# Optimization experiments

Hardware: AMD Instinct MI355X
Metric: run time of the kernel (lower is better)

Reference implementation:

```python
import jax, jax.numpy as jnp
import numpy as np

EPS = 1e-4      # MovingBatchNorm eps
STEPS = 3       # fixed RK4 steps standing in for adaptive dopri5
B, N, D, C, H = 4, 2048, 3, 64, 512


def setup_inputs() -> dict:
    key = jax.random.key(0)
    ks = iter(jax.random.split(key, 40))
    f32 = jnp.float32

    def rn(shape, s=1.0):
        return jax.random.normal(next(ks), shape, dtype=f32) * s

    inp = {}
    inp['x'] = rn((B, N, D))
    inp['c'] = rn((B, N, C))
    for p in ('bn1', 'bn2'):
        inp[p + '_mean'] = rn((D,), 0.1)
        inp[p + '_var'] = jax.random.uniform(next(ks), (D,), dtype=f32, minval=0.5, maxval=1.5)
        inp[p + '_log_gamma'] = jnp.zeros((D,), f32)
        inp[p + '_beta'] = jnp.zeros((D,), f32)
    inp['sqrt_T'] = jnp.array([np.sqrt(0.5)], f32)  # train_T: T = sqrt_T**2
    dims = [(D, H), (H, H), (H, H), (H, D)]  # concatsquash (in, out)
    for i, (din, dout) in enumerate(dims):
        inp[f'W{i}'] = rn((dout, din), 0.05)
        inp[f'b{i}'] = jnp.zeros((dout,), f32)
        inp[f'Wg{i}'] = rn((dout, C + 1), 0.05)
        inp[f'bg{i}'] = jnp.zeros((dout,), f32)
        inp[f'Wb{i}'] = rn((dout, C + 1), 0.05)
    return inp


def _odenet(t, x, c, layers):
    # ConcatSquash MLP: lin(x)*sigmoid(hyper_gate([t,c])) + hyper_bias([t,c])
    ctx = jnp.concatenate([jnp.broadcast_to(t, c.shape[:-1] + (1,)).astype(x.dtype), c], axis=-1)
    h = x
    for i, (W, b, Wg, bg, Wb) in enumerate(layers):
        h = (h @ W.T + b) * jax.nn.sigmoid(ctx @ Wg.T + bg) + ctx @ Wb.T
        if i < len(layers) - 1:
            h = jnp.tanh(h)
    return h


def _aug_dyn(t, x, c, layers):
    # augmented CNF dynamics: (dx/dt, dlogp/dt) with exact divergence via D jvps
    f = lambda xx: _odenet(t, xx, c, layers)
    div = jnp.zeros(x.shape[:-1] + (1,), x.dtype)
    dx = None
    for i in range(x.shape[-1]):
        e = jnp.zeros_like(x).at[..., i].set(1.0)
        dx, jv = jax.jvp(f, (x,), (e,))
        div = div + jv[..., i:i + 1]
    return dx, -div


def _rk4(x0, lp0, c, layers, T):
    dt = T / STEPS

    def step(carry, i):
        x, lp = carry
        t = i.astype(x.dtype) * dt
        k1x, k1l = _aug_dyn(t, x, c, layers)
        k2x, k2l = _aug_dyn(t + 0.5 * dt, x + 0.5 * dt * k1x, c, layers)
        k3x, k3l = _aug_dyn(t + 0.5 * dt, x + 0.5 * dt * k2x, c, layers)
        k4x, k4l = _aug_dyn(t + dt, x + dt * k3x, c, layers)
        x = x + (dt / 6.0) * (k1x + 2.0 * k2x + 2.0 * k3x + k4x)
        lp = lp + (dt / 6.0) * (k1l + 2.0 * k2l + 2.0 * k3l + k4l)
        return (x, lp), None

    (x, lp), _ = jax.lax.scan(step, (x0, lp0), jnp.arange(STEPS))
    return x, lp


def _bn(x, lp, mean, var, log_gamma, beta):
    # MovingBatchNorm1d, eval mode; logdet = sum(log_gamma - 0.5*log(var+eps))
    y = (x - mean) * jnp.exp(log_gamma) / jnp.sqrt(var + EPS) + beta
    ld = jnp.sum(log_gamma - 0.5 * jnp.log(var + EPS))
    return y, lp - ld


def reference(x, c, bn1_mean, bn1_var, bn1_log_gamma, bn1_beta,
              bn2_mean, bn2_var, bn2_log_gamma, bn2_beta, sqrt_T,
              W0, b0, Wg0, bg0, Wb0, W1, b1, Wg1, bg1, Wb1,
              W2, b2, Wg2, bg2, Wb2, W3, b3, Wg3, bg3, Wb3):
    layers = [(W0, b0, Wg0, bg0, Wb0), (W1, b1, Wg1, bg1, Wb1),
              (W2, b2, Wg2, bg2, Wb2), (W3, b3, Wg3, bg3, Wb3)]
    lp = jnp.zeros(x.shape[:-1] + (1,), x.dtype)  # (B,N,1)
    x, lp = _bn(x, lp, bn1_mean, bn1_var, bn1_log_gamma, bn1_beta)
    T = sqrt_T[0] ** 2
    x, lp = _rk4(x, lp, c, layers, T)
    x, lp = _bn(x, lp, bn2_mean, bn2_var, bn2_log_gamma, bn2_beta)
    return x, jnp.sum(lp, axis=(1, 2))
```

## Files before the change

### kernel.cpp

```cpp
#include <hip/hip_runtime.h>
#include <hip/hip_fp8.h>

#define PTS 8192
#define HDIM 512
#define BN_EPS 1e-4f
#define HSTRB 528
#define TS 256.0f
#define SCL1 0x7f7f7f7f

typedef unsigned short u16;
typedef unsigned char u8;
typedef long long i64;
typedef u16 u16x8 __attribute__((ext_vector_type(8)));
typedef short s16x8 __attribute__((ext_vector_type(8)));
typedef float f32x4 __attribute__((ext_vector_type(4)));
typedef float f32x2 __attribute__((ext_vector_type(2)));
typedef int i32x4 __attribute__((ext_vector_type(4)));
typedef int i32x8 __attribute__((ext_vector_type(8)));

__device__ __forceinline__ float bf2f(u16 u) {
  unsigned x = ((unsigned)u) << 16;
  return __builtin_bit_cast(float, x);
}
__device__ __forceinline__ u16 f2bf(float f) {
  unsigned x = __builtin_bit_cast(unsigned, f);
  x += 0x7fffu + ((x >> 16) & 1u);
  return (u16)(x >> 16);
}
__device__ __forceinline__ u8 f2f8(float x) {
  int v = __builtin_amdgcn_cvt_pk_fp8_f32(x, x, 0, false);
  return (u8)(v & 0xff);
}
__device__ __forceinline__ unsigned pk4_f8(float a, float b, float c, float d) {
  int v = __builtin_amdgcn_cvt_pk_fp8_f32(a, b, 0, false);
  v = __builtin_amdgcn_cvt_pk_fp8_f32(c, d, v, true);
  return (unsigned)v;
}
__device__ __forceinline__ float sigf(float x) {
  return __builtin_amdgcn_rcpf(1.f + __expf(-x));
}
__device__ __forceinline__ float fast_tanh(float x) {
  float e = __expf(2.f * x);
  return 1.f - 2.f * __builtin_amdgcn_rcpf(e + 1.f);
}
__device__ __forceinline__ void gl2lds16(const u16* g, u16* l) {
  __builtin_amdgcn_global_load_lds(
      (const __attribute__((address_space(1))) void*)g,
      (__attribute__((address_space(3))) void*)l, 16, 0, 0);
}
__device__ __forceinline__ i32x8 ld32(const u8* p) {
  i32x4 lo = *(const i32x4*)p;
  i32x4 hi = *(const i32x4*)(p + 16);
  return __builtin_shufflevector(lo, hi, 0, 1, 2, 3, 4, 5, 6, 7);
}

#define MFMA_SC(A, B, C) \
  __builtin_amdgcn_mfma_scale_f32_16x16x128_f8f6f4((A), (B), (C), 0, 0, 0, SCL1, 0, SCL1)

#define MX_GEMM(WL, HB)                                                     \
  {                                                                         \
    _Pragma("unroll")                                                       \
    for (int zi = 0; zi < 4; ++zi)                                          \
      _Pragma("unroll")                                                     \
      for (int zj = 0; zj < 4; ++zj)                                        \
        _Pragma("unroll")                                                   \
        for (int zr = 0; zr < 4; ++zr) acc[zi][zj][zr] = 0.f;               \
    const u8* wp = (WL);                                                    \
    _Pragma("unroll 1")                                                     \
    for (int c = 0; c < 4; ++c) {                                           \
      const u8* hc = (HB) + c * 128;                                        \
      i32x8 af0 = ld32(hc);                                                 \
      i32x8 af1 = ld32(hc + (size_t)16 * HSTRB);                            \
      i32x8 af2 = ld32(hc + (size_t)32 * HSTRB);                            \
      i32x8 af3 = ld32(hc + (size_t)48 * HSTRB);                            \
      i32x8 bA = ld32(wp);                                                  \
      i32x8 bB = ld32(wp + 2048);                                           \
      __builtin_amdgcn_sched_barrier(0);                                    \
      __builtin_amdgcn_s_setprio(1);                                        \
      acc[0][0] = MFMA_SC(af0, bA, acc[0][0]);                              \
      acc[1][0] = MFMA_SC(af1, bA, acc[1][0]);                              \
      acc[2][0] = MFMA_SC(af2, bA, acc[2][0]);                              \
      acc[3][0] = MFMA_SC(af3, bA, acc[3][0]);                              \
      acc[0][1] = MFMA_SC(af0, bB, acc[0][1]);                              \
      acc[1][1] = MFMA_SC(af1, bB, acc[1][1]);                              \
      acc[2][1] = MFMA_SC(af2, bB, acc[2][1]);                              \
      acc[3][1] = MFMA_SC(af3, bB, acc[3][1]);                              \
      __builtin_amdgcn_s_setprio(0);                                        \
      __builtin_amdgcn_sched_barrier(0);                                    \
      bA = ld32(wp + 4096);                                                 \
      bB = ld32(wp + 6144);                                                 \
      __builtin_amdgcn_sched_barrier(0);                                    \
      __builtin_amdgcn_s_setprio(1);                                        \
      acc[0][2] = MFMA_SC(af0, bA, acc[0][2]);                              \
      acc[1][2] = MFMA_SC(af1, bA, acc[1][2]);                              \
      acc[2][2] = MFMA_SC(af2, bA, acc[2][2]);                              \
      acc[3][2] = MFMA_SC(af3, bA, acc[3][2]);                              \
      acc[0][3] = MFMA_SC(af0, bB, acc[0][3]);                              \
      acc[1][3] = MFMA_SC(af1, bB, acc[1][3]);                              \
      acc[2][3] = MFMA_SC(af2, bB, acc[2][3]);                              \
      acc[3][3] = MFMA_SC(af3, bB, acc[3][3]);                              \
      __builtin_amdgcn_s_setprio(0);                                        \
      __builtin_amdgcn_sched_barrier(0);                                    \
      wp += 65536;                                                          \
    }                                                                       \
  }

struct PrepArgs {
  const float *W1, *W2;
  u8 *W1s, *W2s;
  const float* c;
  u16* cb;
  const float *Wg0, *Wg1, *Wg2, *Wb0, *Wb1, *Wb2;
  const float *bg0, *bg1, *bg2;
  u16* Wpack;
  float* bias_pack;
  const float *x, *m1, *v1, *lg1, *be1;
  float *x_cur;
  const float *Wg3, *bg3, *Wb3;
  float *G3, *B3;
  const float *W0, *b0, *b1, *b2, *W3;
  float *E0, *E1, *E2;
};
__global__ void prep_kernel(PrepArgs a) {
  int i = blockIdx.x * 256 + threadIdx.x;
  if (i < 512 * 512) {
    int n = i >> 9, k = i & 511;
    int c = k >> 7, q2 = (k >> 5) & 3, b = k & 31;
    int w = n >> 6, j = (n >> 4) & 3, lr = n & 15;
    size_t d = (size_t)c * 65536 + (size_t)w * 8192 + (size_t)j * 2048 +
               (size_t)(q2 * 16 + lr) * 32 + b;
    a.W1s[d] = f2f8(a.W1[i]);
    a.W2s[d] = f2f8(a.W2[i]);
  }
  if (i < PTS * 64) a.cb[i] = f2bf(a.c[i]);
  if (i < 6 * 512 * 64) {
    int sec = i >> 15;
    int within = i & 32767;
    int o = within >> 6, k = within & 63;
    const float* src[6] = {a.Wg0, a.Wg1, a.Wg2, a.Wb0, a.Wb1, a.Wb2};
    a.Wpack[i] = f2bf(src[sec][o * 65 + 1 + k]);
  }
  if (i < 3072) {
    int sec = i >> 9, o = i & 511;
    const float* bgl[3] = {a.bg0, a.bg1, a.bg2};
    a.bias_pack[i] = (sec < 3) ? bgl[sec][o] : 0.f;
  }
  if (i < 512) {
    int o = i;
    a.E0[o * 8 + 0] = a.W0[o * 3];
    a.E0[o * 8 + 1] = a.W0[o * 3 + 1];
    a.E0[o * 8 + 2] = a.W0[o * 3 + 2];
    a.E0[o * 8 + 3] = a.b0[o];
    a.E0[o * 8 + 4] = a.Wg0[o * 65];
    a.E0[o * 8 + 5] = a.Wb0[o * 65];
    a.E0[o * 8 + 6] = 0.f; a.E0[o * 8 + 7] = 0.f;
    a.E1[o * 4 + 0] = a.b1[o];
    a.E1[o * 4 + 1] = a.Wg1[o * 65];
    a.E1[o * 4 + 2] = a.Wb1[o * 65];
    a.E1[o * 4 + 3] = 0.f;
    a.E2[o * 8 + 0] = a.b2[o];
    a.E2[o * 8 + 1] = a.Wg2[o * 65];
    a.E2[o * 8 + 2] = a.Wb2[o * 65];
    a.E2[o * 8 + 3] = a.W3[o];
    a.E2[o * 8 + 4] = a.W3[512 + o];
    a.E2[o * 8 + 5] = a.W3[1024 + o];
    a.E2[o * 8 + 6] = 0.f; a.E2[o * 8 + 7] = 0.f;
  }
  if (i < PTS * 3) {
    int d = i % 3;
    a.x_cur[i] = (a.x[i] - a.m1[d]) * __expf(a.lg1[d]) * rsqrtf(a.v1[d] + BN_EPS) + a.be1[d];
  }
  {
    int lane = threadIdx.x & 63;
    int p = (blockIdx.x * 256 + threadIdx.x) >> 6;
    float cv = a.c[(size_t)p * 64 + lane];
    float ag[3], ab[3];
    #pragma unroll
    for (int o = 0; o < 3; ++o) {
      ag[o] = cv * a.Wg3[o * 65 + 1 + lane];
      ab[o] = cv * a.Wb3[o * 65 + 1 + lane];
    }
    #pragma unroll
    for (int off = 32; off > 0; off >>= 1) {
      #pragma unroll
      for (int o = 0; o < 3; ++o) {
        ag[o] += __shfl_xor(ag[o], off);
        ab[o] += __shfl_xor(ab[o], off);
      }
    }
    if (lane == 0) {
      #pragma unroll
      for (int o = 0; o < 3; ++o) {
        a.G3[p * 3 + o] = ag[o] + a.bg3[o];
        a.B3[p * 3 + o] = ab[o];
      }
    }
  }
}

struct GatesGemmArgs {
  const u16 *A, *W;
  const float* bias;
  u16* GBi;
};
__global__ __launch_bounds__(256) void gates_gemm(GatesGemmArgs a) {
  __shared__ u16 As[128 * 32];
  __shared__ u16 Bs[128 * 32];
  int tid = threadIdx.x;
  int m0 = blockIdx.x * 128, n0 = blockIdx.y * 128;
  int wave = tid >> 6, lane = tid & 63;
  int wm = (wave & 1) * 64, wn = (wave >> 1) * 64;
  int lr = lane & 15, quad = lane >> 4;

  int rowS = tid >> 2, colS = (tid & 3) * 8;
  const u16* gA0 = a.A + (size_t)(m0 + rowS) * 64 + colS;
  const u16* gB0 = a.W + (size_t)(n0 + rowS) * 64 + colS;
  u16* sA0 = &As[tid * 8];
  u16* sA1 = &As[2048 + tid * 8];
  u16* sB0 = &Bs[tid * 8];
  u16* sB1 = &Bs[2048 + tid * 8];

  f32x4 acc[4][4];
  #pragma unroll
  for (int i = 0; i < 4; ++i)
    #pragma unroll
    for (int j = 0; j < 4; ++j)
      #pragma unroll
      for (int r = 0; r < 4; ++r) acc[i][j][r] = 0.f;

  for (int k0 = 0; k0 < 64; k0 += 32) {
    if (k0) __syncthreads();
    gl2lds16(gA0 + k0, sA0);
    gl2lds16(gA0 + (size_t)64 * 64 + k0, sA1);
    gl2lds16(gB0 + k0, sB0);
    gl2lds16(gB0 + (size_t)64 * 64 + k0, sB1);
    __syncthreads();
    s16x8 af[4], bfr[4];
    #pragma unroll
    for (int i = 0; i < 4; ++i)
      af[i] = *(const s16x8*)&As[(wm + i * 16 + lr) * 32 + quad * 8];
    #pragma unroll
    for (int j = 0; j < 4; ++j)
      bfr[j] = *(const s16x8*)&Bs[(wn + j * 16 + lr) * 32 + quad * 8];
    #pragma unroll
    for (int i = 0; i < 4; ++i)
      #pragma unroll
      for (int j = 0; j < 4; ++j)
        acc[i][j] = __builtin_amdgcn_mfma_f32_16x16x32_bf16(af[i], bfr[j], acc[i][j], 0, 0, 0);
  }

  #pragma unroll
  for (int j = 0; j < 4; ++j) {
    int n = n0 + wn + j * 16 + lr;
    int sec = n >> 9, col = n & 511;
    int l = (sec < 3) ? sec : sec - 3;
    int off = col * 2 + ((sec < 3) ? 0 : 1);
    float bv = a.bias[n];
    u16* outp = a.GBi + (size_t)l * PTS * 1024 + off;
    #pragma unroll
    for (int i = 0; i < 4; ++i) {
      int mrow = m0 + wm + i * 16 + quad * 4;
      #pragma unroll
      for (int r = 0; r < 4; ++r)
        outp[(size_t)(mrow + r) * 1024] = f2bf(acc[i][j][r] + bv);
    }
  }
}

struct FlowArgs {
  const float* sqrtT;
  const float *G3, *B3, *Wg3, *Wb3, *b3;
  const float* x0;
  const u16 *GBi0, *GBi1, *GBi2;
  const float *E0, *E1, *E2;
  const u8 *W1s, *W2s;
  const float *m2, *v2, *lg2, *be2;
  float* out_x;
  float* lp_state;
};

__global__ __launch_bounds__(512, 4) void flow_kernel(FlowArgs a) {
  __shared__ __align__(16) u8 HsA[64 * HSTRB];
  __shared__ __align__(16) u8 HsB[64 * HSTRB];
  __shared__ float part[8][16][8];
  __shared__ float xs[2][16][3], kxs[16][3];
  __shared__ float kls[16], lps[16];
  __shared__ float g3s[16][3], b3s[16][3];

  int tid = threadIdx.x;
  int w = tid >> 6, lane = tid & 63, lr = lane & 15, quad = lane >> 4;
  int n0 = w * 64;
  int p0 = blockIdx.x * 16;
  int pl0 = tid >> 5;
  int base_o = (tid & 31) * 16;
  bool desig = (tid & 31) == 0;
  float s0 = a.sqrtT[0];
  float dt = s0 * s0 * (1.f / 3.f);

  const u8* w1l = a.W1s + (size_t)w * 8192 + (size_t)lane * 32;
  const u8* w2l = a.W2s + (size_t)w * 8192 + (size_t)lane * 32;
  const u8* hbA = (const u8*)HsA + (size_t)lr * HSTRB + quad * 32;
  const u8* hbB = (const u8*)HsB + (size_t)lr * HSTRB + quad * 32;

  float wg3r[3], wb3r[3], b3r[3];
  #pragma unroll
  for (int r = 0; r < 3; ++r) {
    wg3r[r] = a.Wg3[r * 65];
    wb3r[r] = a.Wb3[r * 65];
    b3r[r] = a.b3[r];
  }

  const u16* g0p = a.GBi0 + (size_t)(p0 + pl0) * 1024 + 2 * base_o;
  const u16* g1p = a.GBi1 + (size_t)(p0 + quad) * 1024 + 2 * (n0 + lr);
  const u16* g2p = a.GBi2 + (size_t)(p0 + quad) * 1024 + 2 * (n0 + lr);

  if (desig) {
    #pragma unroll
    for (int r = 0; r < 3; ++r) {
      xs[0][pl0][r] = a.x0[(p0 + pl0) * 3 + r];
      g3s[pl0][r] = a.G3[(p0 + pl0) * 3 + r];
      b3s[pl0][r] = a.B3[(p0 + pl0) * 3 + r];
    }
    lps[pl0] = 0.f;
  }
  u16x8 gc0 = *(const u16x8*)(g0p);
  u16x8 gc1 = *(const u16x8*)(g0p + 8);
  u16x8 gc2 = *(const u16x8*)(g0p + 16);
  u16x8 gc3 = *(const u16x8*)(g0p + 24);
  __syncthreads();

  #pragma unroll 1
  for (int s = 0; s < 12; ++s) {
    int sub = s & 3;
    float t = ((float)(s >> 2) + ((sub == 0) ? 0.f : (sub == 3) ? 1.f : 0.5f)) * dt;

    float o0, o1, o2;
    if (s == 0) {
      o0 = xs[0][pl0][0]; o1 = xs[0][pl0][1]; o2 = xs[0][pl0][2];
    } else {
      int m = (s - 1) & 3, q = (s - 1) >> 2;
      float tp = ((float)q + ((m == 0) ? 0.f : (m == 3) ? 1.f : 0.5f)) * dt;
      float fr0 = 0.f, fr1 = 0.f, fr2 = 0.f, fr3 = 0.f, fr4 = 0.f, fr5 = 0.f;
      #pragma unroll
      for (int ww = 0; ww < 8; ++ww) {
        f32x4 pa = *(const f32x4*)&part[ww][pl0][0];
        f32x2 pb = *(const f32x2*)&part[ww][pl0][4];
        fr0 += pa[0]; fr1 += pa[1]; fr2 += pa[2];
        fr3 += pa[3]; fr4 += pb[0]; fr5 += pb[1];
      }
      float ga0 = sigf(g3s[pl0][0] + tp * wg3r[0]);
      float ga1 = sigf(g3s[pl0][1] + tp * wg3r[1]);
      float ga2 = sigf(g3s[pl0][2] + tp * wg3r[2]);
      float dx0 = fmaf(fr0 + b3r[0], ga0, b3s[pl0][0] + tp * wb3r[0]);
      float dx1 = fmaf(fr1 + b3r[1], ga1, b3s[pl0][1] + tp * wb3r[1]);
      float dx2 = fmaf(fr2 + b3r[2], ga2, b3s[pl0][2] + tp * wb3r[2]);
      float klv = -(fr3 * ga0 + fr4 * ga1 + fr5 * ga2);
      float bx0 = xs[q & 1][pl0][0];
      float bx1 = xs[q & 1][pl0][1];
      float bx2 = xs[q & 1][pl0][2];
      if (m == 3) {
        float sc = dt * (1.f / 6.f);
        o0 = bx0 + sc * (kxs[pl0][0] + dx0);
        o1 = bx1 + sc * (kxs[pl0][1] + dx1);
        o2 = bx2 + sc * (kxs[pl0][2] + dx2);
        if (desig) {
          xs[(q + 1) & 1][pl0][0] = o0;
          xs[(q + 1) & 1][pl0][1] = o1;
          xs[(q + 1) & 1][pl0][2] = o2;
          lps[pl0] += sc * (kls[pl0] + klv);
        }
      } else {
        float cf = (m == 2) ? dt : 0.5f * dt;
        o0 = fmaf(cf, dx0, bx0);
        o1 = fmaf(cf, dx1, bx1);
        o2 = fmaf(cf, dx2, bx2);
        if (desig) {
          if (m == 0) {
            kxs[pl0][0] = dx0; kxs[pl0][1] = dx1; kxs[pl0][2] = dx2;
            kls[pl0] = klv;
          } else {
            kxs[pl0][0] += 2.f * dx0; kxs[pl0][1] += 2.f * dx1; kxs[pl0][2] += 2.f * dx2;
            kls[pl0] += 2.f * klv;
          }
        }
      }
    }

    {
      u16x8 gcv[4] = {gc0, gc1, gc2, gc3};
      #pragma unroll
      for (int cc = 0; cc < 4; ++cc) {
        u16x8 v = gcv[cc];
        float hk[4], d0k[4], d1k[4], d2k[4];
        #pragma unroll
        for (int k = 0; k < 4; ++k) {
          int o = base_o + cc * 4 + k;
          f32x4 e = *(const f32x4*)(a.E0 + (size_t)o * 8);
          f32x2 e2 = *(const f32x2*)(a.E0 + (size_t)o * 8 + 4);
          float u = fmaf(e[0], o0, fmaf(e[1], o1, e[2] * o2)) + e[3];
          float gate = sigf(bf2f(v[2 * k]) + t * e2[0]);
          float bias = bf2f(v[2 * k + 1]) + t * e2[1];
          float z = fmaf(u, gate, bias);
          float h = fast_tanh(z);
          float wm = (1.f - h * h) * gate * TS;
          hk[k] = h;
          d0k[k] = wm * e[0];
          d1k[k] = wm * e[1];
          d2k[k] = wm * e[2];
        }
        size_t hbb = (size_t)(pl0 * 4) * HSTRB + base_o + cc * 4;
        *(unsigned*)(HsA + hbb) = pk4_f8(hk[0], hk[1], hk[2], hk[3]);
        *(unsigned*)(HsA + hbb + HSTRB) = pk4_f8(d0k[0], d0k[1], d0k[2], d0k[3]);
        *(unsigned*)(HsA + hbb + 2 * HSTRB) = pk4_f8(d1k[0], d1k[1], d1k[2], d1k[3]);
        *(unsigned*)(HsA + hbb + 3 * HSTRB) = pk4_f8(d2k[0], d2k[1], d2k[2], d2k[3]);
      }
    }
    __syncthreads();

    f32x4 acc[4][4];
    MX_GEMM(w1l, hbA)

    asm("" : "+v"(g1p));
    unsigned g1v[4][4];
    #pragma unroll
    for (int j = 0; j < 4; ++j)
      #pragma unroll
      for (int i = 0; i < 4; ++i)
        g1v[j][i] = *(const unsigned*)(g1p + (size_t)i * 4096 + j * 32);

    #pragma unroll
    for (int j = 0; j < 4; ++j) {
      int n = n0 + j * 16 + lr;
      f32x4 e1 = *(const f32x4*)(a.E1 + (size_t)n * 4);
      #pragma unroll
      for (int i = 0; i < 4; ++i) {
        unsigned d = g1v[j][i];
        float gate = sigf(bf2f((u16)(d & 0xffffu)) + t * e1[1]);
        float bias = bf2f((u16)(d >> 16)) + t * e1[2];
        f32x4 u = acc[i][j];
        float z = fmaf(u[0] + e1[0], gate, bias);
        float h = fast_tanh(z);
        float wmf = (1.f - h * h) * gate;
        int row = i * 16 + quad * 4;
        HsB[(size_t)row * HSTRB + n] = f2f8(h);
        HsB[(size_t)(row + 1) * HSTRB + n] = f2f8(u[1] * wmf);
        HsB[(size_t)(row + 2) * HSTRB + n] = f2f8(u[2] * wmf);
        HsB[(size_t)(row + 3) * HSTRB + n] = f2f8(u[3] * wmf);
      }
    }
    __syncthreads();

    MX_GEMM(w2l, hbB)

    asm("" : "+v"(g2p));
    unsigned g2v[4][4];
    #pragma unroll
    for (int j = 0; j < 4; ++j)
      #pragma unroll
      for (int i = 0; i < 4; ++i)
        g2v[j][i] = *(const unsigned*)(g2p + (size_t)i * 4096 + j * 32);

    asm("" : "+v"(g0p));
    gc0 = *(const u16x8*)(g0p);
    gc1 = *(const u16x8*)(g0p + 8);
    gc2 = *(const u16x8*)(g0p + 16);
    gc3 = *(const u16x8*)(g0p + 24);

    #pragma unroll
    for (int i = 0; i < 4; ++i) {
      float v0 = 0.f, v1 = 0.f, v2 = 0.f, v3 = 0.f, v4 = 0.f, v5 = 0.f;
      int pl = i * 4 + quad;
      #pragma unroll
      for (int j = 0; j < 4; ++j) {
        int n = n0 + j * 16 + lr;
        f32x4 ea = *(const f32x4*)(a.E2 + (size_t)n * 8);
        f32x2 eb = *(const f32x2*)(a.E2 + (size_t)n * 8 + 4);
        unsigned d = g2v[j][i];
        float gate = sigf(bf2f((u16)(d & 0xffffu)) + t * ea[1]);
        float bias = bf2f((u16)(d >> 16)) + t * ea[2];
        f32x4 u = acc[i][j];
        float z = fmaf(u[0] + ea[0], gate, bias);
        float h = fast_tanh(z);
        float wmf = (1.f - h * h) * gate;
        float w30 = ea[3], w31 = eb[0], w32 = eb[1];
        v0 = fmaf(h, w30, v0);
        v1 = fmaf(h, w31, v1);
        v2 = fmaf(h, w32, v2);
        v3 = fmaf(u[1] * wmf, w30, v3);
        v4 = fmaf(u[2] * wmf, w31, v4);
        v5 = fmaf(u[3] * wmf, w32, v5);
      }
      #pragma unroll
      for (int mask = 1; mask <= 8; mask <<= 1) {
        v0 += __shfl_xor(v0, mask);
        v1 += __shfl_xor(v1, mask);
        v2 += __shfl_xor(v2, mask);
        v3 += __shfl_xor(v3, mask);
        v4 += __shfl_xor(v4, mask);
        v5 += __shfl_xor(v5, mask);
      }
      float val = (lr == 0) ? v0 : (lr == 1) ? v1 : (lr == 2) ? v2
                : (lr == 3) ? v3 * (1.f / TS) : (lr == 4) ? v4 * (1.f / TS)
                : v5 * (1.f / TS);
      if (lr < 6) part[w][pl][lr] = val;
    }
    __syncthreads();
  }

  if (desig) {
    int p = p0 + pl0;
    float tp = 3.f * dt;
    float fr0 = 0.f, fr1 = 0.f, fr2 = 0.f, fr3 = 0.f, fr4 = 0.f, fr5 = 0.f;
    #pragma unroll
    for (int ww = 0; ww < 8; ++ww) {
      f32x4 pa = *(const f32x4*)&part[ww][pl0][0];
      f32x2 pb = *(const f32x2*)&part[ww][pl0][4];
      fr0 += pa[0]; fr1 += pa[1]; fr2 += pa[2];
      fr3 += pa[3]; fr4 += pb[0]; fr5 += pb[1];
    }
    float ga0 = sigf(g3s[pl0][0] + tp * wg3r[0]);
    float ga1 = sigf(g3s[pl0][1] + tp * wg3r[1]);
    float ga2 = sigf(g3s[pl0][2] + tp * wg3r[2]);
    float dx[3];
    dx[0] = fmaf(fr0 + b3r[0], ga0, b3s[pl0][0] + tp * wb3r[0]);
    dx[1] = fmaf(fr1 + b3r[1], ga1, b3s[pl0][1] + tp * wb3r[1]);
    dx[2] = fmaf(fr2 + b3r[2], ga2, b3s[pl0][2] + tp * wb3r[2]);
    float klv = -(fr3 * ga0 + fr4 * ga1 + fr5 * ga2);
    float sc = dt * (1.f / 6.f);
    #pragma unroll
    for (int r = 0; r < 3; ++r) {
      float xf = xs[0][pl0][r] + sc * (kxs[pl0][r] + dx[r]);
      a.out_x[p * 3 + r] =
          (xf - a.m2[r]) * __expf(a.lg2[r]) * rsqrtf(a.v2[r] + BN_EPS) + a.be2[r];
    }
    a.lp_state[p] = lps[pl0] + sc * (kls[pl0] + klv);
  }
}

__global__ void finish_lp(const float* __restrict__ lp_state,
                          const float* __restrict__ v1, const float* __restrict__ lg1,
                          const float* __restrict__ v2, const float* __restrict__ lg2,
                          float* __restrict__ out) {
  int b = blockIdx.x, tid = threadIdx.x;
  float s = 0.f;
  for (int n = tid; n < 2048; n += 256) s += lp_state[b * 2048 + n];
  __shared__ float red[256];
  red[tid] = s;
  __syncthreads();
  for (int w = 128; w > 0; w >>= 1) {
    if (tid < w) red[tid] += red[tid + w];
    __syncthreads();
  }
  if (tid == 0) {
    float ld = 0.f;
    for (int d = 0; d < 3; ++d) {
      ld += lg1[d] - 0.5f * logf(v1[d] + BN_EPS);
      ld += lg2[d] - 0.5f * logf(v2[d] + BN_EPS);
    }
    out[b] = red[0] - 2048.f * ld;
  }
}

extern "C" void kernel_launch(void* const* d_in, const int* in_sizes, int n_in,
                              void* d_out, int out_size, void* d_ws, size_t ws_size,
                              hipStream_t stream) {
  const float* x        = (const float*)d_in[0];
  const float* c        = (const float*)d_in[1];
  const float* bn1_mean = (const float*)d_in[2];
  const float* bn1_var  = (const float*)d_in[3];
  const float* bn1_lg   = (const float*)d_in[4];
  const float* bn1_beta = (const float*)d_in[5];
  const float* bn2_mean = (const float*)d_in[6];
  const float* bn2_var  = (const float*)d_in[7];
  const float* bn2_lg   = (const float*)d_in[8];
  const float* bn2_beta = (const float*)d_in[9];
  const float* sqrtT    = (const float*)d_in[10];
  const float* W0  = (const float*)d_in[11];
  const float* b0  = (const float*)d_in[12];
  const float* Wg0 = (const float*)d_in[13];
  const float* bg0 = (const float*)d_in[14];
  const float* Wb0 = (const float*)d_in[15];
  const float* W1  = (const float*)d_in[16];
  const float* b1  = (const float*)d_in[17];
  const float* Wg1 = (const float*)d_in[18];
  const float* bg1 = (const float*)d_in[19];
  const float* Wb1 = (const float*)d_in[20];
  const float* W2  = (const float*)d_in[21];
  const float* b2  = (const float*)d_in[22];
  const float* Wg2 = (const float*)d_in[23];
  const float* bg2 = (const float*)d_in[24];
  const float* Wb2 = (const float*)d_in[25];
  const float* W3  = (const float*)d_in[26];
  const float* b3  = (const float*)d_in[27];
  const float* Wg3 = (const float*)d_in[28];
  const float* bg3 = (const float*)d_in[29];
  const float* Wb3 = (const float*)d_in[30];

  char* base = (char*)d_ws;
  size_t off = 0;
  auto alloc = [&](size_t bytes) -> void* {
    void* pp = base + off;
    off += (bytes + 255) & ~(size_t)255;
    return pp;
  };
  u8* W1s = (u8*)alloc((size_t)512 * 512);
  u8* W2s = (u8*)alloc((size_t)512 * 512);
  u16* cb  = (u16*)alloc((size_t)PTS * 64 * 2);
  u16* Wpack = (u16*)alloc((size_t)6 * 512 * 64 * 2);
  float* bias_pack = (float*)alloc((size_t)3072 * 4);
  u16* GBi = (u16*)alloc((size_t)3 * PTS * 1024 * 2);
  const size_t SZi = (size_t)PTS * 1024;
  u16* GBi0 = GBi;
  u16* GBi1 = GBi + SZi;
  u16* GBi2 = GBi + 2 * SZi;
  float* G3f = (float*)alloc((size_t)PTS * 3 * 4);
  float* B3f = (float*)alloc((size_t)PTS * 3 * 4);
  float* E0 = (float*)alloc((size_t)512 * 8 * 4);
  float* E1 = (float*)alloc((size_t)512 * 4 * 4);
  float* E2 = (float*)alloc((size_t)512 * 8 * 4);
  float* x_cur    = (float*)alloc((size_t)PTS * 3 * 4);
  float* lp_state = (float*)alloc((size_t)PTS * 4);
  (void)ws_size; (void)in_sizes; (void)n_in; (void)out_size;

  PrepArgs pa{W1, W2, W1s, W2s, c, cb, Wg0, Wg1, Wg2, Wb0, Wb1, Wb2,
              bg0, bg1, bg2, Wpack, bias_pack, x, bn1_mean, bn1_var,
              bn1_lg, bn1_beta, x_cur, Wg3, bg3, Wb3, G3f, B3f,
              W0, b0, b1, b2, W3, E0, E1, E2};
  prep_kernel<<<2048, 256, 0, stream>>>(pa);

  GatesGemmArgs gg{cb, Wpack, bias_pack, GBi};
  gates_gemm<<<dim3(64, 24), 256, 0, stream>>>(gg);

  FlowArgs fa{sqrtT, G3f, B3f, Wg3, Wb3, b3, x_cur, GBi0, GBi1, GBi2,
              E0, E1, E2, W1s, W2s, bn2_mean, bn2_var, bn2_lg, bn2_beta,
              (float*)d_out, lp_state};
  flow_kernel<<<PTS / 16, 512, 0, stream>>>(fa);

  finish_lp<<<4, 256, 0, stream>>>(lp_state, bn1_var, bn1_lg, bn2_var, bn2_lg,
                                   (float*)d_out + PTS * 3);
}
```

Baseline: 530.7 us.

## Halve flow-kernel point tile to 8 and split GEMMs into column halves

Each flow block now handles 8 points instead of 16, which doubles the grid and halves LDS buffers. The MX GEMMs and their epilogues run in two column halves so each pass holds a 2x2 accumulator tile instead of 4x4, and launch bounds are raised to allow 6 blocks per CU. The aim is to cut register and LDS pressure so more waves fit and latency is hidden better. In exchange, each weight tile is reused across half as many rows, so weight traffic per point doubles, and there are more per-block overheads.

```diff
diff --git a/kernel.cpp b/kernel.cpp
--- a/kernel.cpp
+++ b/kernel.cpp
@@ -57,51 +57,116 @@
 #define MFMA_SC(A, B, C) \
   __builtin_amdgcn_mfma_scale_f32_16x16x128_f8f6f4((A), (B), (C), 0, 0, 0, SCL1, 0, SCL1)
 
-#define MX_GEMM(WL, HB)                                                     \
+#define MX_HALF(WL, HB, H)                                                  \
   {                                                                         \
     _Pragma("unroll")                                                       \
-    for (int zi = 0; zi < 4; ++zi)                                          \
+    for (int zi = 0; zi < 2; ++zi)                                          \
       _Pragma("unroll")                                                     \
-      for (int zj = 0; zj < 4; ++zj)                                        \
+      for (int zj = 0; zj < 2; ++zj)                                        \
         _Pragma("unroll")                                                   \
         for (int zr = 0; zr < 4; ++zr) acc[zi][zj][zr] = 0.f;               \
-    const u8* wp = (WL);                                                    \
+    const u8* wp = (WL) + (H) * 4096;                                       \
     _Pragma("unroll 1")                                                     \
     for (int c = 0; c < 4; ++c) {                                           \
       const u8* hc = (HB) + c * 128;                                        \
       i32x8 af0 = ld32(hc);                                                 \
       i32x8 af1 = ld32(hc + (size_t)16 * HSTRB);                            \
-      i32x8 af2 = ld32(hc + (size_t)32 * HSTRB);                            \
-      i32x8 af3 = ld32(hc + (size_t)48 * HSTRB);                            \
       i32x8 bA = ld32(wp);                                                  \
       i32x8 bB = ld32(wp + 2048);                                           \
       __builtin_amdgcn_sched_barrier(0);                                    \
       __builtin_amdgcn_s_setprio(1);                                        \
       acc[0][0] = MFMA_SC(af0, bA, acc[0][0]);                              \
       acc[1][0] = MFMA_SC(af1, bA, acc[1][0]);                              \
-      acc[2][0] = MFMA_SC(af2, bA, acc[2][0]);                              \
-      acc[3][0] = MFMA_SC(af3, bA, acc[3][0]);                              \
       acc[0][1] = MFMA_SC(af0, bB, acc[0][1]);                              \
       acc[1][1] = MFMA_SC(af1, bB, acc[1][1]);                              \
-      acc[2][1] = MFMA_SC(af2, bB, acc[2][1]);                              \
-      acc[3][1] = MFMA_SC(af3, bB, acc[3][1]);                              \
-      __builtin_amdgcn_s_setprio(0);                                        \
-      __builtin_amdgcn_sched_barrier(0);                                    \
-      bA = ld32(wp + 4096);                                                 \
-      bB = ld32(wp + 6144);                                                 \
-      __builtin_amdgcn_sched_barrier(0);                                    \
-      __builtin_amdgcn_s_setprio(1);                                        \
-      acc[0][2] = MFMA_SC(af0, bA, acc[0][2]);                              \
-      acc[1][2] = MFMA_SC(af1, bA, acc[1][2]);                              \
-      acc[2][2] = MFMA_SC(af2, bA, acc[2][2]);                              \
-      acc[3][2] = MFMA_SC(af3, bA, acc[3][2]);                              \
-      acc[0][3] = MFMA_SC(af0, bB, acc[0][3]);                              \
-      acc[1][3] = MFMA_SC(af1, bB, acc[1][3]);                              \
-      acc[2][3] = MFMA_SC(af2, bB, acc[2][3]);                              \
-      acc[3][3] = MFMA_SC(af3, bB, acc[3][3]);                              \
       __builtin_amdgcn_s_setprio(0);                                        \
       __builtin_amdgcn_sched_barrier(0);                                    \
       wp += 65536;                                                          \
+    }                                                                       \
+  }
+
+#define EPI1_HALF(H)                                                        \
+  {                                                                         \
+    asm("" : "+v"(g1p));                                                    \
+    unsigned g1v[2][2];                                                     \
+    _Pragma("unroll")                                                       \
+    for (int jl = 0; jl < 2; ++jl)                                          \
+      _Pragma("unroll")                                                     \
+      for (int i = 0; i < 2; ++i)                                           \
+        g1v[jl][i] = *(const unsigned*)(g1p + (size_t)i * 4096 +            \
+                                        ((H) * 2 + jl) * 32);               \
+    _Pragma("unroll")                                                       \
+    for (int jl = 0; jl < 2; ++jl) {                                        \
+      int n = n0 + ((H) * 2 + jl) * 16 + lr;                                \
+      f32x4 e1 = *(const f32x4*)(a.E1 + (size_t)n * 4);                     \
+      _Pragma("unroll")                                                     \
+      for (int i = 0; i < 2; ++i) {                                         \
+        unsigned d = g1v[jl][i];                                            \
+        float gate = sigf(bf2f((u16)(d & 0xffffu)) + t * e1[1]);            \
+        float bias = bf2f((u16)(d >> 16)) + t * e1[2];                      \
+        f32x4 u = acc[i][jl];                                               \
+        float z = fmaf(u[0] + e1[0], gate, bias);                           \
+        float hh = fast_tanh(z);                                            \
+        float wmf = (1.f - hh * hh) * gate;                                 \
+        int row = i * 16 + quad * 4;                                        \
+        HsB[(size_t)row * HSTRB + n] = f2f8(hh);                            \
+        HsB[(size_t)(row + 1) * HSTRB + n] = f2f8(u[1] * wmf);              \
+        HsB[(size_t)(row + 2) * HSTRB + n] = f2f8(u[2] * wmf);              \
+        HsB[(size_t)(row + 3) * HSTRB + n] = f2f8(u[3] * wmf);              \
+      }                                                                     \
+    }                                                                       \
+  }
+
+#define EPI2_HALF(H)                                                        \
+  {                                                                         \
+    asm("" : "+v"(g2p));                                                    \
+    unsigned g2v[2][2];                                                     \
+    _Pragma("unroll")                                                       \
+    for (int jl = 0; jl < 2; ++jl)                                          \
+      _Pragma("unroll")                                                     \
+      for (int i = 0; i < 2; ++i)                                           \
+        g2v[jl][i] = *(const unsigned*)(g2p + (size_t)i * 4096 +            \
+                                        ((H) * 2 + jl) * 32);               \
+    _Pragma("unroll")                                                       \
+    for (int i = 0; i < 2; ++i) {                                           \
+      float v0 = 0.f, v1 = 0.f, v2 = 0.f, v3 = 0.f, v4 = 0.f, v5 = 0.f;     \
+      _Pragma("unroll")                                                     \
+      for (int jl = 0; jl < 2; ++jl) {                                      \
+        int n = n0 + ((H) * 2 + jl) * 16 + lr;                              \
+        f32x4 ea = *(const f32x4*)(a.E2 + (size_t)n * 8);                   \
+        f32x2 eb = *(const f32x2*)(a.E2 + (size_t)n * 8 + 4);               \
+        unsigned d = g2v[jl][i];                                            \
+        float gate = sigf(bf2f((u16)(d & 0xffffu)) + t * ea[1]);            \
+        float bias = bf2f((u16)(d >> 16)) + t * ea[2];                      \
+        f32x4 u = acc[i][jl];                                               \
+        float z = fmaf(u[0] + ea[0], gate, bias);                           \
+        float hh = fast_tanh(z);                                            \
+        float wmf = (1.f - hh * hh) * gate;                                 \
+        float w30 = ea[3], w31 = eb[0], w32 = eb[1];                        \
+        v0 = fmaf(hh, w30, v0);                                             \
+        v1 = fmaf(hh, w31, v1);                                             \
+        v2 = fmaf(hh, w32, v2);                                             \
+        v3 = fmaf(u[1] * wmf, w30, v3);                                     \
+        v4 = fmaf(u[2] * wmf, w31, v4);                                     \
+        v5 = fmaf(u[3] * wmf, w32, v5);                                     \
+      }                                                                     \
+      _Pragma("unroll")                                                     \
+      for (int mask = 1; mask <= 8; mask <<= 1) {                           \
+        v0 += __shfl_xor(v0, mask);                                         \
+        v1 += __shfl_xor(v1, mask);                                         \
+        v2 += __shfl_xor(v2, mask);                                         \
+        v3 += __shfl_xor(v3, mask);                                         \
+        v4 += __shfl_xor(v4, mask);                                         \
+        v5 += __shfl_xor(v5, mask);                                         \
+      }                                                                     \
+      float val = (lr == 0) ? v0 : (lr == 1) ? v1 : (lr == 2) ? v2          \
+                : (lr == 3) ? v3 * (1.f / TS) : (lr == 4) ? v4 * (1.f / TS) \
+                : v5 * (1.f / TS);                                          \
+      int pl = i * 4 + quad;                                                \
+      if (lr < 6) {                                                         \
+        if ((H) == 0) part[w][pl][lr] = val;                                \
+        else part[w][pl][lr] += val;                                        \
+      }                                                                     \
     }                                                                       \
   }
 
@@ -279,21 +344,21 @@
   float* lp_state;
 };
 
-__global__ __launch_bounds__(512, 4) void flow_kernel(FlowArgs a) {
-  __shared__ __align__(16) u8 HsA[64 * HSTRB];
-  __shared__ __align__(16) u8 HsB[64 * HSTRB];
-  __shared__ float part[8][16][8];
-  __shared__ float xs[2][16][3], kxs[16][3];
-  __shared__ float kls[16], lps[16];
-  __shared__ float g3s[16][3], b3s[16][3];
+__global__ __launch_bounds__(512, 6) void flow_kernel(FlowArgs a) {
+  __shared__ __align__(16) u8 HsA[32 * HSTRB];
+  __shared__ __align__(16) u8 HsB[32 * HSTRB];
+  __shared__ float part[8][8][8];
+  __shared__ float xs[2][8][3], kxs[8][3];
+  __shared__ float kls[8], lps[8];
+  __shared__ float g3s[8][3], b3s[8][3];
 
   int tid = threadIdx.x;
   int w = tid >> 6, lane = tid & 63, lr = lane & 15, quad = lane >> 4;
   int n0 = w * 64;
-  int p0 = blockIdx.x * 16;
-  int pl0 = tid >> 5;
-  int base_o = (tid & 31) * 16;
-  bool desig = (tid & 31) == 0;
+  int p0 = blockIdx.x * 8;
+  int pl0 = tid >> 6;
+  int base_o = (tid & 63) * 8;
+  bool desig = (tid & 63) == 0;
   float s0 = a.sqrtT[0];
   float dt = s0 * s0 * (1.f / 3.f);
 
@@ -325,8 +390,6 @@
   }
   u16x8 gc0 = *(const u16x8*)(g0p);
   u16x8 gc1 = *(const u16x8*)(g0p + 8);
-  u16x8 gc2 = *(const u16x8*)(g0p + 16);
-  u16x8 gc3 = *(const u16x8*)(g0p + 24);
   __syncthreads();
 
   #pragma unroll 1
@@ -387,9 +450,9 @@
     }
 
     {
-      u16x8 gcv[4] = {gc0, gc1, gc2, gc3};
+      u16x8 gcv[2] = {gc0, gc1};
       #pragma unroll
-      for (int cc = 0; cc < 4; ++cc) {
+      for (int cc = 0; cc < 2; ++cc) {
         u16x8 v = gcv[cc];
         float hk[4], d0k[4], d1k[4], d2k[4];
         #pragma unroll
@@ -417,93 +480,20 @@
     }
     __syncthreads();
 
-    f32x4 acc[4][4];
-    MX_GEMM(w1l, hbA)
-
-    asm("" : "+v"(g1p));
-    unsigned g1v[4][4];
-    #pragma unroll
-    for (int j = 0; j < 4; ++j)
-      #pragma unroll
-      for (int i = 0; i < 4; ++i)
-        g1v[j][i] = *(const unsigned*)(g1p + (size_t)i * 4096 + j * 32);
-
-    #pragma unroll
-    for (int j = 0; j < 4; ++j) {
-      int n = n0 + j * 16 + lr;
-      f32x4 e1 = *(const f32x4*)(a.E1 + (size_t)n * 4);
-      #pragma unroll
-      for (int i = 0; i < 4; ++i) {
-        unsigned d = g1v[j][i];
-        float gate = sigf(bf2f((u16)(d & 0xffffu)) + t * e1[1]);
-        float bias = bf2f((u16)(d >> 16)) + t * e1[2];
-        f32x4 u = acc[i][j];
-        float z = fmaf(u[0] + e1[0], gate, bias);
-        float h = fast_tanh(z);
-        float wmf = (1.f - h * h) * gate;
-        int row = i * 16 + quad * 4;
-        HsB[(size_t)row * HSTRB + n] = f2f8(h);
-        HsB[(size_t)(row + 1) * HSTRB + n] = f2f8(u[1] * wmf);
-        HsB[(size_t)(row + 2) * HSTRB + n] = f2f8(u[2] * wmf);
-        HsB[(size_t)(row + 3) * HSTRB + n] = f2f8(u[3] * wmf);
-      }
-    }
+    f32x4 acc[2][2];
+    MX_HALF(w1l, hbA, 0)
+    EPI1_HALF(0)
+    MX_HALF(w1l, hbA, 1)
+    EPI1_HALF(1)
     __syncthreads();
 
-    MX_GEMM(w2l, hbB)
-
-    asm("" : "+v"(g2p));
-    unsigned g2v[4][4];
-    #pragma unroll
-    for (int j = 0; j < 4; ++j)
-      #pragma unroll
-      for (int i = 0; i < 4; ++i)
-        g2v[j][i] = *(const unsigned*)(g2p + (size_t)i * 4096 + j * 32);
-
+    MX_HALF(w2l, hbB, 0)
+    EPI2_HALF(0)
+    MX_HALF(w2l, hbB, 1)
     asm("" : "+v"(g0p));
     gc0 = *(const u16x8*)(g0p);
     gc1 = *(const u16x8*)(g0p + 8);
-    gc2 = *(const u16x8*)(g0p + 16);
-    gc3 = *(const u16x8*)(g0p + 24);
-
-    #pragma unroll
-    for (int i = 0; i < 4; ++i) {
-      float v0 = 0.f, v1 = 0.f, v2 = 0.f, v3 = 0.f, v4 = 0.f, v5 = 0.f;
-      int pl = i * 4 + quad;
-      #pragma unroll
-      for (int j = 0; j < 4; ++j) {
-        int n = n0 + j * 16 + lr;
-        f32x4 ea = *(const f32x4*)(a.E2 + (size_t)n * 8);
-        f32x2 eb = *(const f32x2*)(a.E2 + (size_t)n * 8 + 4);
-        unsigned d = g2v[j][i];
-        float gate = sigf(bf2f((u16)(d & 0xffffu)) + t * ea[1]);
-        float bias = bf2f((u16)(d >> 16)) + t * ea[2];
-        f32x4 u = acc[i][j];
-        float z = fmaf(u[0] + ea[0], gate, bias);
-        float h = fast_tanh(z);
-        float wmf = (1.f - h * h) * gate;
-        float w30 = ea[3], w31 = eb[0], w32 = eb[1];
-        v0 = fmaf(h, w30, v0);
-        v1 = fmaf(h, w31, v1);
-        v2 = fmaf(h, w32, v2);
-        v3 = fmaf(u[1] * wmf, w30, v3);
-        v4 = fmaf(u[2] * wmf, w31, v4);
-        v5 = fmaf(u[3] * wmf, w32, v5);
-      }
-      #pragma unroll
-      for (int mask = 1; mask <= 8; mask <<= 1) {
-        v0 += __shfl_xor(v0, mask);
-        v1 += __shfl_xor(v1, mask);
-        v2 += __shfl_xor(v2, mask);
-        v3 += __shfl_xor(v3, mask);
-        v4 += __shfl_xor(v4, mask);
-        v5 += __shfl_xor(v5, mask);
-      }
-      float val = (lr == 0) ? v0 : (lr == 1) ? v1 : (lr == 2) ? v2
-                : (lr == 3) ? v3 * (1.f / TS) : (lr == 4) ? v4 * (1.f / TS)
-                : v5 * (1.f / TS);
-      if (lr < 6) part[w][pl][lr] = val;
-    }
+    EPI2_HALF(1)
     __syncthreads();
   }
 
@@ -634,7 +624,7 @@
   FlowArgs fa{sqrtT, G3f, B3f, Wg3, Wb3, b3, x_cur, GBi0, GBi1, GBi2,
               E0, E1, E2, W1s, W2s, bn2_mean, bn2_var, bn2_lg, bn2_beta,
               (float*)d_out, lp_state};
-  flow_kernel<<<PTS / 16, 512, 0, stream>>>(fa);
+  flow_kernel<<<PTS / 8, 512, 0, stream>>>(fa);
 
   finish_lp<<<4, 256, 0, stream>>>(lp_state, bn1_var, bn1_lg, bn2_var, bn2_lg,
                                    (float*)d_out + PTS * 3);
```

Measured after the change: 643.2 us. 1.21x slower.
